# Performance work log

Measured on AMD Instinct MI355X. Metric: run time of the kernel, lower is better.

The kernel has to match this reference:

```python
import jax, jax.numpy as jnp
import numpy as np

L, DM, H, DK, DV, DFF = 4, 1024, 16, 64, 64, 4096
B, T, S = 4, 1024, 1024
EPS = 1e-5


def layer_norm(x):
    m = jnp.mean(x, axis=-1, keepdims=True)
    v = jnp.mean((x - m) ** 2, axis=-1, keepdims=True)
    return (x - m) / jnp.sqrt(v + EPS)


def mha(x_q, x_kv, Wq, Wk, Wv, Wo, mask):
    # x_q: [B,Lq,DM], x_kv: [B,Lk,DM], W*: [DM, H*DK] (pre-transposed), Wo: [H*DV, DM]
    b, lq, _ = x_q.shape
    lk = x_kv.shape[1]
    Q = (x_q @ Wq).reshape(b, lq, H, DK).transpose(0, 2, 1, 3)   # [B,H,Lq,DK]
    K = (x_kv @ Wk).reshape(b, lk, H, DK).transpose(0, 2, 1, 3)
    V = (x_kv @ Wv).reshape(b, lk, H, DV).transpose(0, 2, 1, 3)
    scores = jnp.einsum('bhqd,bhkd->bhqk', Q, K) / np.sqrt(DK).astype(np.float32)
    scores = jnp.where(mask[:, None, :, :], jnp.float32(-1e9), scores)  # masked_fill_
    attn = jax.nn.softmax(scores, axis=-1)
    ctx = jnp.einsum('bhqk,bhkv->bqhv', attn, V).reshape(b, lq, H * DV)
    out = ctx @ Wo
    return layer_norm(out + x_q)


def ffn(x, W1, W2):
    return layer_norm(jax.nn.relu(x @ W1) @ W2 + x)


def setup_inputs() -> dict:
    key = jax.random.key(0)
    ks = jax.random.split(key, 12)
    sc = 0.02
    inp = {
        'dec_inputs': jax.random.normal(ks[0], (B, T, DM), jnp.float32),
        'enc_outputs': jax.random.normal(ks[1], (B, S, DM), jnp.float32),
        # causal mask per get_attn_subsequence_mask (True = masked)
        'dec_self_attn_mask': jnp.broadcast_to(jnp.triu(jnp.ones((T, T), bool), k=1), (B, T, T)),
        'dec_enc_attn_mask': jnp.zeros((B, T, S), bool),
        'self_Wq': sc * jax.random.normal(ks[2], (L, DM, H * DK), jnp.float32),
        'self_Wk': sc * jax.random.normal(ks[3], (L, DM, H * DK), jnp.float32),
        'self_Wv': sc * jax.random.normal(ks[4], (L, DM, H * DV), jnp.float32),
        'self_Wo': sc * jax.random.normal(ks[5], (L, H * DV, DM), jnp.float32),
        'cross_Wq': sc * jax.random.normal(ks[6], (L, DM, H * DK), jnp.float32),
        'cross_Wk': sc * jax.random.normal(ks[7], (L, DM, H * DK), jnp.float32),
        'cross_Wv': sc * jax.random.normal(ks[8], (L, DM, H * DV), jnp.float32),
        'cross_Wo': sc * jax.random.normal(ks[9], (L, H * DV, DM), jnp.float32),
        'ffn_W1': sc * jax.random.normal(ks[10], (L, DM, DFF), jnp.float32),
        'ffn_W2': sc * jax.random.normal(ks[11], (L, DFF, DM), jnp.float32),
    }
    return inp


def reference(dec_inputs, enc_outputs, dec_self_attn_mask, dec_enc_attn_mask,
              self_Wq, self_Wk, self_Wv, self_Wo,
              cross_Wq, cross_Wk, cross_Wv, cross_Wo,
              ffn_W1, ffn_W2):
    x = dec_inputs
    for l in range(L):  # fixed small layer count
        x = mha(x, x, self_Wq[l], self_Wk[l], self_Wv[l], self_Wo[l], dec_self_attn_mask)
        x = mha(x, enc_outputs, cross_Wq[l], cross_Wk[l], cross_Wv[l], cross_Wo[l], dec_enc_attn_mask)
        x = ffn(x, ffn_W1[l], ffn_W2[l])
    return x
```

## Files before the change

kernel.cpp:

```cpp
#include <hip/hip_runtime.h>

typedef unsigned short u16;
typedef unsigned int u32;
typedef __bf16 bf16x8 __attribute__((ext_vector_type(8)));
typedef float f32x4 __attribute__((ext_vector_type(4)));

#define TT 1024

__device__ __forceinline__ u16 f2bf(float f) {
  u32 u = __float_as_uint(f);
  u32 r = (u + 0x7fffu + ((u >> 16) & 1u)) >> 16;
  return (u16)r;
}
__device__ __forceinline__ float bf2f(u16 b) {
  return __uint_as_float(((u32)b) << 16);
}

__device__ __forceinline__ void gl_lds16(const void* g, void* l) {
  __builtin_amdgcn_global_load_lds(
      (const __attribute__((address_space(1))) u32*)g,
      (__attribute__((address_space(3))) u32*)l, 16, 0, 0);
}

__global__ __launch_bounds__(256) void k_f32_to_bf16(const float* __restrict__ in,
                                                     u16* __restrict__ out, int n) {
  int i = (blockIdx.x * 256 + threadIdx.x) * 4;
  if (i >= n) return;
  float4 v = *(const float4*)(in + i);
  ushort4 o;
  o.x = f2bf(v.x); o.y = f2bf(v.y); o.z = f2bf(v.z); o.w = f2bf(v.w);
  *(ushort4*)(out + i) = o;
}

__global__ __launch_bounds__(256) void k_init(const float* __restrict__ in,
                                              u16* __restrict__ bfo,
                                              float* __restrict__ fo, int n) {
  int i = (blockIdx.x * 256 + threadIdx.x) * 4;
  if (i >= n) return;
  float4 v = *(const float4*)(in + i);
  ushort4 o;
  o.x = f2bf(v.x); o.y = f2bf(v.y); o.z = f2bf(v.z); o.w = f2bf(v.w);
  *(ushort4*)(bfo + i) = o;
  *(float4*)(fo + i) = v;
}

struct TPack {
  const float* src[8];
  u16* dst[8];
};
__global__ __launch_bounds__(256) void k_transpose(TPack p, int R, int C) {
  __shared__ float tile[32][33];
  const int tx = threadIdx.x & 31;
  const int ty = threadIdx.x >> 5;
  const float* __restrict__ src = p.src[blockIdx.z];
  u16* __restrict__ dst = p.dst[blockIdx.z];
  const int c0 = blockIdx.x * 32;
  const int r0 = blockIdx.y * 32;
#pragma unroll
  for (int i = 0; i < 4; i++)
    tile[ty + i * 8][tx] = src[(size_t)(r0 + ty + i * 8) * C + c0 + tx];
  __syncthreads();
#pragma unroll
  for (int i = 0; i < 4; i++)
    dst[(size_t)(c0 + ty + i * 8) * R + r0 + tx] = f2bf(tile[tx][ty + i * 8]);
}

__global__ __launch_bounds__(256) void k_tbf(const u16* __restrict__ src, int ld,
                                             u16* __restrict__ dst) {
  __shared__ u16 tile[32][33];
  const int r0 = blockIdx.y * 32;
  const int c0 = blockIdx.x * 32;
  const int tr = threadIdx.x >> 3;
  const int tc = (threadIdx.x & 7) * 4;
  ushort4 v = *(const ushort4*)&src[(size_t)(r0 + tr) * ld + c0 + tc];
  tile[tr][tc] = v.x; tile[tr][tc + 1] = v.y; tile[tr][tc + 2] = v.z; tile[tr][tc + 3] = v.w;
  __syncthreads();
  ushort4 o;
  o.x = tile[tc][tr]; o.y = tile[tc + 1][tr]; o.z = tile[tc + 2][tr]; o.w = tile[tc + 3][tr];
  *(ushort4*)&dst[(size_t)(c0 + tr) * 4096 + r0 + tc] = o;
}

template <int OUT_BF16, int RELU, int SPLITK>
__global__ __launch_bounds__(256) void k_gemm_tn(const u16* __restrict__ A,
                                                 const u16* __restrict__ Bt,
                                                 void* __restrict__ Cout,
                                                 void* __restrict__ Cout2,
                                                 int M, int N, int K) {
  __shared__ __attribute__((aligned(16))) u16 sA[2][128 * 32];
  __shared__ __attribute__((aligned(16))) u16 sB[2][128 * 32];
  const int tid = threadIdx.x;
  const int wave = tid >> 6;
  const int lane = tid & 63;
  const int quad = lane >> 4;
  const int lc = lane & 15;
  const int m0 = blockIdx.x * 128;
  const int n0 = blockIdx.y * 128;
  const int wr = (wave >> 1) * 64;
  const int wc = (wave & 1) * 64;

  const int Ks = K / SPLITK;
  const size_t kOff = (size_t)blockIdx.z * Ks;

  const int c0 = wave * 2, c1 = wave * 2 + 1;
  const int srow = lane >> 2;
  const int scol = ((lane & 3) ^ ((srow >> 1) & 3)) * 8;

  const u16* a0 = A + (size_t)(m0 + c0 * 16 + srow) * K + kOff + scol;
  const u16* a1 = A + (size_t)(m0 + c1 * 16 + srow) * K + kOff + scol;
  const u16* b0 = Bt + (size_t)(n0 + c0 * 16 + srow) * K + kOff + scol;
  const u16* b1 = Bt + (size_t)(n0 + c1 * 16 + srow) * K + kOff + scol;

  f32x4 acc[4][4];
  const f32x4 z4 = {0.f, 0.f, 0.f, 0.f};
#pragma unroll
  for (int i = 0; i < 4; i++)
#pragma unroll
    for (int j = 0; j < 4; j++) acc[i][j] = z4;

  const int qs = quad ^ ((lc >> 1) & 3);

  auto stage = [&](int buf) {
    gl_lds16(a0, &sA[buf][c0 * 512]);
    gl_lds16(a1, &sA[buf][c1 * 512]);
    gl_lds16(b0, &sB[buf][c0 * 512]);
    gl_lds16(b1, &sB[buf][c1 * 512]);
    a0 += 32; a1 += 32; b0 += 32; b1 += 32;
  };

  stage(0);
  int cur = 0;
  for (int k0 = 0; k0 < Ks; k0 += 32) {
    __syncthreads();
    if (k0 + 32 < Ks) stage(cur ^ 1);
    bf16x8 af[4], bfr[4];
#pragma unroll
    for (int i = 0; i < 4; i++)
      af[i] = *(const bf16x8*)&sA[cur][(wr + i * 16 + lc) * 32 + qs * 8];
#pragma unroll
    for (int j = 0; j < 4; j++)
      bfr[j] = *(const bf16x8*)&sB[cur][(wc + j * 16 + lc) * 32 + qs * 8];
#pragma unroll
    for (int i = 0; i < 4; i++)
#pragma unroll
      for (int j = 0; j < 4; j++)
        acc[i][j] = __builtin_amdgcn_mfma_f32_16x16x32_bf16(af[i], bfr[j], acc[i][j], 0, 0, 0);
    cur ^= 1;
  }

  void* Cw = (SPLITK > 1 && blockIdx.z == 1) ? Cout2 : Cout;
#pragma unroll
  for (int i = 0; i < 4; i++) {
    const int row = m0 + wr + i * 16 + quad * 4;
#pragma unroll
    for (int j = 0; j < 4; j++) {
      const int col = n0 + wc + j * 16 + lc;
#pragma unroll
      for (int r = 0; r < 4; r++) {
        float v = acc[i][j][r];
        if (RELU) v = fmaxf(v, 0.f);
        if (OUT_BF16)
          ((u16*)Cw)[(size_t)(row + r) * N + col] = f2bf(v);
        else
          ((float*)Cw)[(size_t)(row + r) * N + col] = v;
      }
    }
  }
}

template <int CAUSAL>
__global__ __launch_bounds__(256, 4) void k_flash(const u16* __restrict__ Q, int ldq,
                                                  const u16* __restrict__ K, int ldk,
                                                  const u16* __restrict__ Vt,
                                                  u16* __restrict__ O) {
  __shared__ __attribute__((aligned(16))) u16 sK[2][64 * 64];
  __shared__ __attribute__((aligned(16))) u16 sV[2][64 * 64];
  __shared__ __attribute__((aligned(16))) u16 sP[4][16 * 64];
  const int tid = threadIdx.x;
  const int wave = tid >> 6;
  const int lane = tid & 63;
  const int quad = lane >> 4;
  const int lc = lane & 15;
  const int qb = blockIdx.x;
  const int b = blockIdx.y >> 4;
  const int h = blockIdx.y & 15;
  const size_t rowB = (size_t)b * TT;
  const int qrow = qb * 64 + wave * 16;
  const int hc = h * 64;

  const bf16x8 qf0 = *(const bf16x8*)&Q[(rowB + qrow + lc) * ldq + hc + quad * 8];
  const bf16x8 qf1 = *(const bf16x8*)&Q[(rowB + qrow + lc) * ldq + hc + 32 + quad * 8];

  f32x4 o[4];
  float m_r[4], l_r[4];
  const f32x4 z4 = {0.f, 0.f, 0.f, 0.f};
#pragma unroll
  for (int d = 0; d < 4; d++) o[d] = z4;
#pragma unroll
  for (int r = 0; r < 4; r++) { m_r[r] = -1e30f; l_r[r] = 0.f; }

  const float cvt = 1.4426950408889634f / 8.0f;
  u16* myP = sP[wave];
  const int l7 = lc & 7;
  const int swr = (lc >> 2) | ((lc & 1) << 2);
  const int p_lo = wave * 64 + lane;

  const int nkt = CAUSAL ? (qb + 1) : 16;

  auto stage = [&](int cur, int s0) {
#pragma unroll
    for (int half = 0; half < 2; half++) {
      const int p = half * 256 + p_lo;
      const int row = p >> 3;
      const int cb = (p & 7) ^ (row & 7);
      const int p0 = half * 256 + wave * 64;
      gl_lds16(K + (rowB + s0 + row) * (size_t)ldk + hc + cb * 8, &sK[cur][p0 * 8]);
      gl_lds16(Vt + (size_t)(hc + row) * 4096 + rowB + s0 + cb * 8, &sV[cur][p0 * 8]);
    }
  };

  stage(0, 0);
  int cur = 0;
  for (int kt = 0; kt < nkt; kt++) {
    const int s0 = kt * 64;
    __syncthreads();
    if (kt + 1 < nkt) stage(cur ^ 1, s0 + 64);

    f32x4 s[4];
#pragma unroll
    for (int st = 0; st < 4; st++) {
      const int key = st * 16 + lc;
      const bf16x8 kf0 = *(const bf16x8*)&sK[cur][key * 64 + ((quad ^ l7) * 8)];
      const bf16x8 kf1 = *(const bf16x8*)&sK[cur][key * 64 + (((4 + quad) ^ l7) * 8)];
      f32x4 z = z4;
      z = __builtin_amdgcn_mfma_f32_16x16x32_bf16(qf0, kf0, z, 0, 0, 0);
      z = __builtin_amdgcn_mfma_f32_16x16x32_bf16(qf1, kf1, z, 0, 0, 0);
      s[st] = z;
    }

#pragma unroll
    for (int r = 0; r < 4; r++) {
      float sv0 = s[0][r] * cvt, sv1 = s[1][r] * cvt;
      float sv2 = s[2][r] * cvt, sv3 = s[3][r] * cvt;
      if (CAUSAL) {
        const int qg = qrow + quad * 4 + r;
        if (s0 + lc > qg) sv0 = -1e30f;
        if (s0 + 16 + lc > qg) sv1 = -1e30f;
        if (s0 + 32 + lc > qg) sv2 = -1e30f;
        if (s0 + 48 + lc > qg) sv3 = -1e30f;
      }
      float pm = fmaxf(fmaxf(sv0, sv1), fmaxf(sv2, sv3));
      pm = fmaxf(pm, __shfl_xor(pm, 1));
      pm = fmaxf(pm, __shfl_xor(pm, 2));
      pm = fmaxf(pm, __shfl_xor(pm, 4));
      pm = fmaxf(pm, __shfl_xor(pm, 8));
      const float mn = fmaxf(m_r[r], pm);
      const float al = exp2f(m_r[r] - mn);
      m_r[r] = mn;
      const float p0 = exp2f(sv0 - mn);
      const float p1 = exp2f(sv1 - mn);
      const float p2 = exp2f(sv2 - mn);
      const float p3 = exp2f(sv3 - mn);
      l_r[r] = l_r[r] * al + (p0 + p1 + p2 + p3);
      const int row = quad * 4 + r;
      const int sw = quad | ((r & 1) << 2);
      u16* pr = myP + row * 64 + l7;
      pr[(((lc >> 3) | 0) ^ sw) * 8] = f2bf(p0);
      pr[(((lc >> 3) | 2) ^ sw) * 8] = f2bf(p1);
      pr[(((lc >> 3) | 4) ^ sw) * 8] = f2bf(p2);
      pr[(((lc >> 3) | 6) ^ sw) * 8] = f2bf(p3);
#pragma unroll
      for (int d = 0; d < 4; d++) o[d][r] *= al;
    }

#pragma unroll
    for (int c = 0; c < 2; c++) {
      const bf16x8 pf = *(const bf16x8*)&myP[lc * 64 + (((c * 4 + quad) ^ swr) * 8)];
#pragma unroll
      for (int d = 0; d < 4; d++) {
        const int dv = d * 16 + lc;
        const bf16x8 vf = *(const bf16x8*)&sV[cur][dv * 64 + (((c * 4 + quad) ^ l7) * 8)];
        o[d] = __builtin_amdgcn_mfma_f32_16x16x32_bf16(pf, vf, o[d], 0, 0, 0);
      }
    }
    cur ^= 1;
  }

#pragma unroll
  for (int r = 0; r < 4; r++) {
    float l = l_r[r];
    l += __shfl_xor(l, 1);
    l += __shfl_xor(l, 2);
    l += __shfl_xor(l, 4);
    l += __shfl_xor(l, 8);
    const float inv = 1.0f / l;
    const size_t orow = (rowB + qrow + quad * 4 + r) * 1024 + hc;
#pragma unroll
    for (int d = 0; d < 4; d++) O[orow + d * 16 + lc] = f2bf(o[d][r] * inv);
  }
}

template <int NSUM>
__global__ __launch_bounds__(256) void k_ln(const float* __restrict__ y0,
                                            const float* __restrict__ y1,
                                            float* __restrict__ xf,
                                            u16* __restrict__ xb,
                                            float* __restrict__ fout) {
  const int row = blockIdx.x;
  const int tid = threadIdx.x;
  const int lane = tid & 63, wave = tid >> 6;
  const size_t base = (size_t)row * 1024 + tid * 4;
  float4 v = *(const float4*)&y0[base];
  float4 xv = *(const float4*)&xf[base];
  if (NSUM == 2) {
    float4 w = *(const float4*)&y1[base];
    v.x += w.x; v.y += w.y; v.z += w.z; v.w += w.w;
  }
  v.x += xv.x; v.y += xv.y; v.z += xv.z; v.w += xv.w;
  float s = v.x + v.y + v.z + v.w;
  float ss = v.x * v.x + v.y * v.y + v.z * v.z + v.w * v.w;
#pragma unroll
  for (int off = 1; off < 64; off <<= 1) {
    s += __shfl_xor(s, off);
    ss += __shfl_xor(ss, off);
  }
  __shared__ float rs[4], rss[4];
  if (lane == 0) { rs[wave] = s; rss[wave] = ss; }
  __syncthreads();
  const float S = rs[0] + rs[1] + rs[2] + rs[3];
  const float SS = rss[0] + rss[1] + rss[2] + rss[3];
  const float mean = S * (1.f / 1024.f);
  const float var = SS * (1.f / 1024.f) - mean * mean;
  const float inv = rsqrtf(var + 1e-5f);
  const float o0 = (v.x - mean) * inv, o1 = (v.y - mean) * inv;
  const float o2 = (v.z - mean) * inv, o3 = (v.w - mean) * inv;
  float4 fo; fo.x = o0; fo.y = o1; fo.z = o2; fo.w = o3;
  *(float4*)&xf[base] = fo;
  ushort4 ob;
  ob.x = f2bf(o0); ob.y = f2bf(o1); ob.z = f2bf(o2); ob.w = f2bf(o3);
  *(ushort4*)&xb[base] = ob;
  if (fout) *(float4*)&fout[base] = fo;
}

extern "C" void kernel_launch(void* const* d_in, const int* in_sizes, int n_in,
                              void* d_out, int out_size, void* d_ws, size_t ws_size,
                              hipStream_t stream) {
  const float* dec_inputs  = (const float*)d_in[0];
  const float* enc_outputs = (const float*)d_in[1];
  const float* self_Wq = (const float*)d_in[4];
  const float* self_Wk = (const float*)d_in[5];
  const float* self_Wv = (const float*)d_in[6];
  const float* self_Wo = (const float*)d_in[7];
  const float* cross_Wq = (const float*)d_in[8];
  const float* cross_Wk = (const float*)d_in[9];
  const float* cross_Wv = (const float*)d_in[10];
  const float* cross_Wo = (const float*)d_in[11];
  const float* ffn_W1 = (const float*)d_in[12];
  const float* ffn_W2 = (const float*)d_in[13];

  char* ws = (char*)d_ws;
  const size_t MB = 1024 * 1024;
  u16* wq_t = (u16*)(ws + 0 * MB);
  u16* wk_t = (u16*)(ws + 2 * MB);
  u16* wv_t = (u16*)(ws + 4 * MB);
  u16* wo_t = (u16*)(ws + 6 * MB);
  u16* cq_t = (u16*)(ws + 8 * MB);
  u16* ck_t = (u16*)(ws + 10 * MB);
  u16* cv_t = (u16*)(ws + 12 * MB);
  u16* co_t = (u16*)(ws + 14 * MB);
  u16* w1_t = (u16*)(ws + 16 * MB);
  u16* w2_t = (u16*)(ws + 24 * MB);
  u16* encb = (u16*)(ws + 32 * MB);
  u16* xb   = (u16*)(ws + 40 * MB);
  u16* qkv  = (u16*)(ws + 48 * MB);
  u16* kvb  = (u16*)(ws + 56 * MB);
  u16* ctx  = (u16*)(ws + 72 * MB);
  u16* hbuf = (u16*)(ws + 48 * MB);
  float* yb = (float*)(ws + 80 * MB);
  u16* vtb  = (u16*)(ws + 80 * MB);
  float* xf = (float*)(ws + 96 * MB);
  float* ysA = (float*)(ws + 48 * MB);
  float* ysW = (float*)(ws + 0 * MB);

  const int NTOK = 4 * TT * 1024;

  k_init<<<4096, 256, 0, stream>>>(dec_inputs, xb, xf, NTOK);
  k_f32_to_bf16<<<4096, 256, 0, stream>>>(enc_outputs, encb, NTOK);

  for (int l = 0; l < 4; l++) {
    const size_t sqOff = (size_t)l * 1024 * 1024;
    const size_t ffOff = (size_t)l * 4096 * 1024;
    TPack sq;
    sq.src[0] = self_Wq + sqOff;  sq.dst[0] = wq_t;
    sq.src[1] = self_Wk + sqOff;  sq.dst[1] = wk_t;
    sq.src[2] = self_Wv + sqOff;  sq.dst[2] = wv_t;
    sq.src[3] = self_Wo + sqOff;  sq.dst[3] = wo_t;
    sq.src[4] = cross_Wq + sqOff; sq.dst[4] = cq_t;
    sq.src[5] = cross_Wk + sqOff; sq.dst[5] = ck_t;
    sq.src[6] = cross_Wv + sqOff; sq.dst[6] = cv_t;
    sq.src[7] = cross_Wo + sqOff; sq.dst[7] = co_t;
    k_transpose<<<dim3(32, 32, 8), 256, 0, stream>>>(sq, 1024, 1024);
    TPack p1 = sq; p1.src[0] = ffn_W1 + ffOff; p1.dst[0] = w1_t;
    k_transpose<<<dim3(128, 32, 1), 256, 0, stream>>>(p1, 1024, 4096);
    TPack p2 = sq; p2.src[0] = ffn_W2 + ffOff; p2.dst[0] = w2_t;
    k_transpose<<<dim3(32, 128, 1), 256, 0, stream>>>(p2, 4096, 1024);

    k_gemm_tn<1, 0, 1><<<dim3(32, 24), 256, 0, stream>>>(xb, wq_t, qkv, nullptr, 4096, 3072, 1024);
    k_tbf<<<dim3(32, 128), 256, 0, stream>>>(qkv + 2048, 3072, vtb);
    k_flash<1><<<dim3(16, 64), 256, 0, stream>>>(qkv, 3072, qkv + 1024, 3072, vtb, ctx);
    k_gemm_tn<0, 0, 2><<<dim3(32, 8, 2), 256, 0, stream>>>(ctx, wo_t, yb, ysA, 4096, 1024, 1024);
    k_ln<2><<<4096, 256, 0, stream>>>(yb, ysA, xf, xb, nullptr);

    k_gemm_tn<1, 0, 1><<<dim3(32, 8), 256, 0, stream>>>(xb, cq_t, qkv, nullptr, 4096, 1024, 1024);
    k_gemm_tn<1, 0, 1><<<dim3(32, 16), 256, 0, stream>>>(encb, ck_t, kvb, nullptr, 4096, 2048, 1024);
    k_tbf<<<dim3(32, 128), 256, 0, stream>>>(kvb + 1024, 2048, vtb);
    k_flash<0><<<dim3(16, 64), 256, 0, stream>>>(qkv, 1024, kvb, 2048, vtb, ctx);
    k_gemm_tn<0, 0, 2><<<dim3(32, 8, 2), 256, 0, stream>>>(ctx, co_t, yb, ysA, 4096, 1024, 1024);
    k_ln<2><<<4096, 256, 0, stream>>>(yb, ysA, xf, xb, nullptr);

    k_gemm_tn<1, 1, 1><<<dim3(32, 32), 256, 0, stream>>>(xb, w1_t, hbuf, nullptr, 4096, 4096, 1024);
    k_gemm_tn<0, 0, 2><<<dim3(32, 8, 2), 256, 0, stream>>>(hbuf, w2_t, yb, ysW, 4096, 1024, 4096);
    k_ln<2><<<4096, 256, 0, stream>>>(yb, ysW, xf, xb, (l == 3) ? (float*)d_out : nullptr);
  }
}
```

Baseline: 1.865 ms.

## Widen flash-attention blocks to 128 query rows and remap blocks across XCDs

The flash attention kernel now runs 8 waves per block covering 128 query rows, so each staged K/V tile in LDS is shared by twice as many query rows. Each thread issues one K and one V LDS load per tile instead of two, halving global-to-LDS traffic per query. A 1D grid is remapped so blocks from the same batch/head land on the same XCD, which should improve L2 reuse of K/V. The cost is fewer blocks (512) and coarser causal granularity: on the diagonal tiles half the waves compute masked work, and larger blocks may lower occupancy.

```diff
diff --git a/kernel.cpp b/kernel.cpp
--- a/kernel.cpp
+++ b/kernel.cpp
@@ -168,23 +168,27 @@
 }
 
 template <int CAUSAL>
-__global__ __launch_bounds__(256, 4) void k_flash(const u16* __restrict__ Q, int ldq,
+__global__ __launch_bounds__(512, 6) void k_flash(const u16* __restrict__ Q, int ldq,
                                                   const u16* __restrict__ K, int ldk,
                                                   const u16* __restrict__ Vt,
                                                   u16* __restrict__ O) {
   __shared__ __attribute__((aligned(16))) u16 sK[2][64 * 64];
   __shared__ __attribute__((aligned(16))) u16 sV[2][64 * 64];
-  __shared__ __attribute__((aligned(16))) u16 sP[4][16 * 64];
+  __shared__ __attribute__((aligned(16))) u16 sP[8][16 * 64];
   const int tid = threadIdx.x;
   const int wave = tid >> 6;
   const int lane = tid & 63;
   const int quad = lane >> 4;
   const int lc = lane & 15;
-  const int qb = blockIdx.x;
-  const int b = blockIdx.y >> 4;
-  const int h = blockIdx.y & 15;
+  const int id = blockIdx.x;
+  const int xcd = id & 7;
+  const int s_ = id >> 3;
+  const int y = xcd * 8 + (s_ >> 3);
+  const int qb = s_ & 7;
+  const int b = y >> 4;
+  const int h = y & 15;
   const size_t rowB = (size_t)b * TT;
-  const int qrow = qb * 64 + wave * 16;
+  const int qrow = qb * 128 + wave * 16;
   const int hc = h * 64;
 
   const bf16x8 qf0 = *(const bf16x8*)&Q[(rowB + qrow + lc) * ldq + hc + quad * 8];
@@ -202,20 +206,16 @@
   u16* myP = sP[wave];
   const int l7 = lc & 7;
   const int swr = (lc >> 2) | ((lc & 1) << 2);
-  const int p_lo = wave * 64 + lane;
-
-  const int nkt = CAUSAL ? (qb + 1) : 16;
+
+  const int nkt = CAUSAL ? (2 * qb + 2) : 16;
+
+  const int prow = tid >> 3;
+  const int pcb = (tid & 7) ^ (prow & 7);
+  const int p0 = wave * 64;
 
   auto stage = [&](int cur, int s0) {
-#pragma unroll
-    for (int half = 0; half < 2; half++) {
-      const int p = half * 256 + p_lo;
-      const int row = p >> 3;
-      const int cb = (p & 7) ^ (row & 7);
-      const int p0 = half * 256 + wave * 64;
-      gl_lds16(K + (rowB + s0 + row) * (size_t)ldk + hc + cb * 8, &sK[cur][p0 * 8]);
-      gl_lds16(Vt + (size_t)(hc + row) * 4096 + rowB + s0 + cb * 8, &sV[cur][p0 * 8]);
-    }
+    gl_lds16(K + (rowB + s0 + prow) * (size_t)ldk + hc + pcb * 8, &sK[cur][p0 * 8]);
+    gl_lds16(Vt + (size_t)(hc + prow) * 4096 + rowB + s0 + pcb * 8, &sV[cur][p0 * 8]);
   };
 
   stage(0, 0);
@@ -256,18 +256,18 @@
       const float mn = fmaxf(m_r[r], pm);
       const float al = exp2f(m_r[r] - mn);
       m_r[r] = mn;
-      const float p0 = exp2f(sv0 - mn);
-      const float p1 = exp2f(sv1 - mn);
-      const float p2 = exp2f(sv2 - mn);
-      const float p3 = exp2f(sv3 - mn);
-      l_r[r] = l_r[r] * al + (p0 + p1 + p2 + p3);
+      const float p0_ = exp2f(sv0 - mn);
+      const float p1_ = exp2f(sv1 - mn);
+      const float p2_ = exp2f(sv2 - mn);
+      const float p3_ = exp2f(sv3 - mn);
+      l_r[r] = l_r[r] * al + (p0_ + p1_ + p2_ + p3_);
       const int row = quad * 4 + r;
       const int sw = quad | ((r & 1) << 2);
       u16* pr = myP + row * 64 + l7;
-      pr[(((lc >> 3) | 0) ^ sw) * 8] = f2bf(p0);
-      pr[(((lc >> 3) | 2) ^ sw) * 8] = f2bf(p1);
-      pr[(((lc >> 3) | 4) ^ sw) * 8] = f2bf(p2);
-      pr[(((lc >> 3) | 6) ^ sw) * 8] = f2bf(p3);
+      pr[(((lc >> 3) | 0) ^ sw) * 8] = f2bf(p0_);
+      pr[(((lc >> 3) | 2) ^ sw) * 8] = f2bf(p1_);
+      pr[(((lc >> 3) | 4) ^ sw) * 8] = f2bf(p2_);
+      pr[(((lc >> 3) | 6) ^ sw) * 8] = f2bf(p3_);
 #pragma unroll
       for (int d = 0; d < 4; d++) o[d][r] *= al;
     }
@@ -406,14 +406,14 @@
 
     k_gemm_tn<1, 0, 1><<<dim3(32, 24), 256, 0, stream>>>(xb, wq_t, qkv, nullptr, 4096, 3072, 1024);
     k_tbf<<<dim3(32, 128), 256, 0, stream>>>(qkv + 2048, 3072, vtb);
-    k_flash<1><<<dim3(16, 64), 256, 0, stream>>>(qkv, 3072, qkv + 1024, 3072, vtb, ctx);
+    k_flash<1><<<512, 512, 0, stream>>>(qkv, 3072, qkv + 1024, 3072, vtb, ctx);
     k_gemm_tn<0, 0, 2><<<dim3(32, 8, 2), 256, 0, stream>>>(ctx, wo_t, yb, ysA, 4096, 1024, 1024);
     k_ln<2><<<4096, 256, 0, stream>>>(yb, ysA, xf, xb, nullptr);
 
     k_gemm_tn<1, 0, 1><<<dim3(32, 8), 256, 0, stream>>>(xb, cq_t, qkv, nullptr, 4096, 1024, 1024);
     k_gemm_tn<1, 0, 1><<<dim3(32, 16), 256, 0, stream>>>(encb, ck_t, kvb, nullptr, 4096, 2048, 1024);
     k_tbf<<<dim3(32, 128), 256, 0, stream>>>(kvb + 1024, 2048, vtb);
-    k_flash<0><<<dim3(16, 64), 256, 0, stream>>>(qkv, 1024, kvb, 2048, vtb, ctx);
+    k_flash<0><<<512, 512, 0, stream>>>(qkv, 1024, kvb, 2048, vtb, ctx);
     k_gemm_tn<0, 0, 2><<<dim3(32, 8, 2), 256, 0, stream>>>(ctx, co_t, yb, ysA, 4096, 1024, 1024);
     k_ln<2><<<4096, 256, 0, stream>>>(yb, ysA, xf, xb, nullptr);
 
```

After: 1.953 ms. +4.7%, slower.
